# Kernel optimization log

Measured on AMD Instinct MI355X. Metric: run time of the kernel, lower is better.

Reference implementation:

```python
import jax, jax.numpy as jnp
import numpy as np

NEG_SLOPE = 0.01  # torch F.leaky_relu default
EPS = 1e-12


def setup_inputs() -> dict:
    key = jax.random.key(0)
    k1, k2, k3, k4 = jax.random.split(key, 4)
    num_nodes, in_f, out_f, num_edges = 50000, 128, 128, 600000
    x = jax.random.normal(k1, (num_nodes, in_f), dtype=jnp.float32)
    edge_index = jax.random.randint(k2, (2, num_edges), 0, num_nodes, dtype=jnp.int64)
    # xavier_uniform for W:[out,in]
    limit = float(np.sqrt(6.0 / (in_f + out_f)))
    W = jax.random.uniform(k3, (out_f, in_f), dtype=jnp.float32, minval=-limit, maxval=limit)
    a = jax.random.uniform(k4, (2 * out_f,), dtype=jnp.float32, minval=0.0, maxval=1.0)
    return {"x": x, "edge_index": edge_index, "W": W, "a": a}


def reference(x, edge_index, W, a):
    num_nodes = x.shape[0]
    out_f = W.shape[0]
    # add self loops
    loops = jnp.arange(num_nodes, dtype=edge_index.dtype)
    src = jnp.concatenate([edge_index[0], loops])
    dst = jnp.concatenate([edge_index[1], loops])
    messages = x @ W.T                      # [N, F_out]
    # cat([h_src,h_dst]) @ a == h_src @ a[:F] + h_dst @ a[F:] (avoids materializing concat)
    s_src = messages @ a[:out_f]            # [N]
    s_dst = messages @ a[out_f:]            # [N]
    e_ij = jax.nn.leaky_relu(s_src[src] + s_dst[dst], negative_slope=NEG_SLOPE)  # [E]
    w = jnp.exp(e_ij)                       # unnormalized edge weights
    denom = jax.ops.segment_sum(w, dst, num_segments=num_nodes)
    denom = jnp.maximum(denom, EPS)
    weighted = w[:, None] * messages[src]   # [E, F_out]
    agg = jax.ops.segment_sum(weighted, dst, num_segments=num_nodes)
    return agg / denom[:, None]
```

## Files before the change

### kernel.cpp

```cpp
#include <hip/hip_runtime.h>

#define NEG_SLOPE 0.01f
#define CAP 64

typedef __attribute__((ext_vector_type(8))) short bf16x8;
typedef __attribute__((ext_vector_type(4))) float f32x4;

static __device__ __forceinline__ unsigned short f2bf(float f) {
  unsigned u = __float_as_uint(f);
  u += 0x7fffu + ((u >> 16) & 1u);
  return (unsigned short)(u >> 16);
}

__global__ __launch_bounds__(256) void k_setup(const float* __restrict__ W,
                                               const float* __restrict__ a,
                                               unsigned short* __restrict__ Wb,
                                               float* __restrict__ p_lo,
                                               float* __restrict__ p_hi,
                                               int* __restrict__ counts, int N, int nz) {
  int b = blockIdx.x;
  int t = threadIdx.x;
  if (b < nz) {
    int i = b * 256 + t;
    if (i < N) counts[i] = 0;
  } else if (b < nz + 64) {
    int i = (b - nz) * 256 + t;
    Wb[i] = f2bf(W[i]);
  } else {
    if (t < 128) {
      float lo = 0.f, hi = 0.f;
#pragma unroll 8
      for (int f = 0; f < 128; ++f) {
        float w = W[f * 128 + t];
        lo += w * a[f];
        hi += w * a[128 + f];
      }
      p_lo[t] = lo;
      p_hi[t] = hi;
    }
  }
}

__global__ __launch_bounds__(256) void k_msg(const float* __restrict__ x,
                                             const float* __restrict__ p_lo,
                                             const float* __restrict__ p_hi,
                                             const unsigned short* __restrict__ Wb,
                                             unsigned short* __restrict__ msgs,
                                             float* __restrict__ s_src,
                                             float* __restrict__ s_dst, int N) {
  int wave = (blockIdx.x * 256 + threadIdx.x) >> 6;
  int lane = threadIdx.x & 63;
  int base = wave * 16;
  if (base >= N) return;
  int q = lane >> 4, r = lane & 15;
  int node = base + r;
  const float* xrow = x + (size_t)node * 128 + q * 8;
  const float4* pl = (const float4*)p_lo;
  const float4* ph = (const float4*)p_hi;
  bf16x8 afrag[4];
  float lo = 0.f, hi = 0.f;
#pragma unroll
  for (int c = 0; c < 4; ++c) {
    float4 v0 = *(const float4*)(xrow + c * 32);
    float4 v1 = *(const float4*)(xrow + c * 32 + 4);
    int fi = q * 2 + c * 8;
    float4 a0 = pl[fi], a1 = pl[fi + 1];
    float4 b0 = ph[fi], b1 = ph[fi + 1];
    lo += v0.x * a0.x + v0.y * a0.y + v0.z * a0.z + v0.w * a0.w
        + v1.x * a1.x + v1.y * a1.y + v1.z * a1.z + v1.w * a1.w;
    hi += v0.x * b0.x + v0.y * b0.y + v0.z * b0.z + v0.w * b0.w
        + v1.x * b1.x + v1.y * b1.y + v1.z * b1.z + v1.w * b1.w;
    bf16x8 f;
    f[0] = (short)f2bf(v0.x); f[1] = (short)f2bf(v0.y);
    f[2] = (short)f2bf(v0.z); f[3] = (short)f2bf(v0.w);
    f[4] = (short)f2bf(v1.x); f[5] = (short)f2bf(v1.y);
    f[6] = (short)f2bf(v1.z); f[7] = (short)f2bf(v1.w);
    afrag[c] = f;
  }
  lo += __shfl_xor(lo, 16); lo += __shfl_xor(lo, 32);
  hi += __shfl_xor(hi, 16); hi += __shfl_xor(hi, 32);
  if (q == 0) { s_src[node] = lo; s_dst[node] = hi; }
#pragma unroll
  for (int ft = 0; ft < 8; ++ft) {
    const unsigned short* wrow = Wb + (size_t)(ft * 16 + r) * 128 + q * 8;
    f32x4 acc = {0.f, 0.f, 0.f, 0.f};
#pragma unroll
    for (int c = 0; c < 4; ++c) {
      bf16x8 bfrag = *(const bf16x8*)(wrow + c * 32);
      acc = __builtin_amdgcn_mfma_f32_16x16x32_bf16(afrag[c], bfrag, acc, 0, 0, 0);
    }
#pragma unroll
    for (int rr = 0; rr < 4; ++rr) {
      int n2 = base + q * 4 + rr;
      msgs[(size_t)n2 * 128 + ft * 16 + r] = f2bf(acc[rr]);
    }
  }
}

__global__ __launch_bounds__(256) void k_scatter(const int* __restrict__ ei,
                                                 const float* __restrict__ s_src,
                                                 const float* __restrict__ s_dst,
                                                 int* __restrict__ counts,
                                                 int2* __restrict__ edges, int E) {
  int e2 = blockIdx.x * 256 + threadIdx.x;
  int e = e2 * 2;
  if (e >= E) return;
  int2 srcp = *(const int2*)(ei + e);
  int2 dstp = *(const int2*)(ei + E + e);
  {
    float z = s_src[srcp.x] + s_dst[dstp.x];
    z = z > 0.f ? z : NEG_SLOPE * z;
    float w = expf(z);
    int pos = atomicAdd(&counts[dstp.x], 1);
    if (pos < CAP) edges[(size_t)dstp.x * CAP + pos] = make_int2(srcp.x, __float_as_int(w));
  }
  if (e + 1 < E) {
    float z = s_src[srcp.y] + s_dst[dstp.y];
    z = z > 0.f ? z : NEG_SLOPE * z;
    float w = expf(z);
    int pos = atomicAdd(&counts[dstp.y], 1);
    if (pos < CAP) edges[(size_t)dstp.y * CAP + pos] = make_int2(srcp.y, __float_as_int(w));
  }
}

__global__ __launch_bounds__(256) void k_agg(const unsigned short* __restrict__ msgs,
                                             const int* __restrict__ counts,
                                             const int2* __restrict__ edges,
                                             const float* __restrict__ s_src,
                                             const float* __restrict__ s_dst,
                                             float* __restrict__ out, int N) {
  int wave = (blockIdx.x * 256 + threadIdx.x) >> 6;
  int lane = threadIdx.x & 63;
  if (wave >= N) return;
  int node = wave;
  int g = lane >> 4;
  int r = lane & 15;
  float zs = s_src[node] + s_dst[node];
  zs = zs > 0.f ? zs : NEG_SLOPE * zs;
  float wself = expf(zs);
  float wg = (g == 0) ? wself : 0.f;
  float denom = wg;
  float acc[8];
  {
    const uint4* mrow = (const uint4*)(msgs + (size_t)node * 128);
    uint4 m = mrow[r];
    unsigned mm[4] = {m.x, m.y, m.z, m.w};
#pragma unroll
    for (int c = 0; c < 4; ++c) {
      acc[2 * c]     = wg * __uint_as_float(mm[c] << 16);
      acc[2 * c + 1] = wg * __uint_as_float(mm[c] & 0xffff0000u);
    }
  }
  int cnt = counts[node];
  cnt = cnt < CAP ? cnt : CAP;
  const int2* bucket = edges + (size_t)node * CAP;
  int nIter = (cnt + 7) >> 3;
  for (int it = 0; it < nIter; ++it) {
    int k0 = it * 8 + g;
    int k1 = k0 + 4;
    bool v0 = k0 < cnt, v1 = k1 < cnt;
    int2 e0 = bucket[v0 ? k0 : 0];
    int2 e1 = bucket[v1 ? k1 : 0];
    float w0 = v0 ? __int_as_float(e0.y) : 0.f;
    float w1 = v1 ? __int_as_float(e1.y) : 0.f;
    uint4 m0 = ((const uint4*)(msgs + (size_t)e0.x * 128))[r];
    uint4 m1 = ((const uint4*)(msgs + (size_t)e1.x * 128))[r];
    unsigned a0[4] = {m0.x, m0.y, m0.z, m0.w};
    unsigned a1[4] = {m1.x, m1.y, m1.z, m1.w};
#pragma unroll
    for (int c = 0; c < 4; ++c) {
      acc[2 * c]     += w0 * __uint_as_float(a0[c] << 16);
      acc[2 * c + 1] += w0 * __uint_as_float(a0[c] & 0xffff0000u);
      acc[2 * c]     += w1 * __uint_as_float(a1[c] << 16);
      acc[2 * c + 1] += w1 * __uint_as_float(a1[c] & 0xffff0000u);
    }
    denom += w0 + w1;
  }
#pragma unroll
  for (int mask = 16; mask < 64; mask <<= 1) {
#pragma unroll
    for (int j = 0; j < 8; ++j) acc[j] += __shfl_xor(acc[j], mask);
    denom += __shfl_xor(denom, mask);
  }
  if (g == 0) {
    float inv = 1.f / fmaxf(denom, 1e-12f);
    float4 o0 = {acc[0] * inv, acc[1] * inv, acc[2] * inv, acc[3] * inv};
    float4 o1 = {acc[4] * inv, acc[5] * inv, acc[6] * inv, acc[7] * inv};
    float4* orow = (float4*)(out + (size_t)node * 128);
    orow[r * 2] = o0;
    orow[r * 2 + 1] = o1;
  }
}

extern "C" void kernel_launch(void* const* d_in, const int* in_sizes, int n_in,
                              void* d_out, int out_size, void* d_ws, size_t ws_size,
                              hipStream_t stream) {
  const float* x = (const float*)d_in[0];
  const int* ei = (const int*)d_in[1];
  const float* W = (const float*)d_in[2];
  const float* a = (const float*)d_in[3];
  float* out = (float*)d_out;
  int N = in_sizes[0] / 128;
  int E = in_sizes[1] / 2;

  char* ws = (char*)d_ws;
  size_t off = 0;
  auto alloc = [&](size_t bytes) {
    off = (off + 255) & ~(size_t)255;
    void* p = ws + off;
    off += bytes;
    return p;
  };
  unsigned short* msgs = (unsigned short*)alloc((size_t)N * 128 * 2);
  float* s_src = (float*)alloc((size_t)N * 4);
  float* s_dst = (float*)alloc((size_t)N * 4);
  float* p_lo = (float*)alloc(512);
  float* p_hi = (float*)alloc(512);
  unsigned short* Wb = (unsigned short*)alloc(128 * 128 * 2);
  int* counts = (int*)alloc((size_t)N * 4);
  int2* edges = (int2*)alloc((size_t)N * CAP * 8);

  int nz = (N + 255) / 256;
  int waves = (N + 15) / 16;
  k_setup<<<nz + 64 + 1, 256, 0, stream>>>(W, a, Wb, p_lo, p_hi, counts, N, nz);
  k_msg<<<(waves + 3) / 4, 256, 0, stream>>>(x, p_lo, p_hi, Wb, msgs, s_src, s_dst, N);
  int e2 = (E + 1) / 2;
  k_scatter<<<(e2 + 255) / 256, 256, 0, stream>>>(ei, s_src, s_dst, counts, edges, E);
  k_agg<<<(N + 3) / 4, 256, 0, stream>>>(msgs, counts, edges, s_src, s_dst, out, N);
}
```

Before: 165.9 us.

## Move edge weight computation into aggregation and shrink edge buckets to indices

The scatter kernel now stores only the source index per bucket slot instead of an (index, weight) pair, which halves the bucket storage and its write and read traffic. The attention weight (gather s_src, leaky relu, exp) is recomputed inside the aggregation kernel per edge. Scatter no longer depends on s_src and s_dst, so it is launched before the message kernel. The cost is an extra random s_src gather and an exp per edge in the aggregation loop.

After: 164.6 us. No clear change (-0.8%).

```diff
diff --git a/kernel.cpp b/kernel.cpp
--- a/kernel.cpp
+++ b/kernel.cpp
@@ -98,34 +98,24 @@
 }
 
 __global__ __launch_bounds__(256) void k_scatter(const int* __restrict__ ei,
-                                                 const float* __restrict__ s_src,
-                                                 const float* __restrict__ s_dst,
                                                  int* __restrict__ counts,
-                                                 int2* __restrict__ edges, int E) {
+                                                 unsigned* __restrict__ edges, int E) {
   int e2 = blockIdx.x * 256 + threadIdx.x;
   int e = e2 * 2;
   if (e >= E) return;
   int2 srcp = *(const int2*)(ei + e);
   int2 dstp = *(const int2*)(ei + E + e);
-  {
-    float z = s_src[srcp.x] + s_dst[dstp.x];
-    z = z > 0.f ? z : NEG_SLOPE * z;
-    float w = expf(z);
-    int pos = atomicAdd(&counts[dstp.x], 1);
-    if (pos < CAP) edges[(size_t)dstp.x * CAP + pos] = make_int2(srcp.x, __float_as_int(w));
-  }
+  int pos0 = atomicAdd(&counts[dstp.x], 1);
+  if (pos0 < CAP) edges[(size_t)dstp.x * CAP + pos0] = (unsigned)srcp.x;
   if (e + 1 < E) {
-    float z = s_src[srcp.y] + s_dst[dstp.y];
-    z = z > 0.f ? z : NEG_SLOPE * z;
-    float w = expf(z);
-    int pos = atomicAdd(&counts[dstp.y], 1);
-    if (pos < CAP) edges[(size_t)dstp.y * CAP + pos] = make_int2(srcp.y, __float_as_int(w));
+    int pos1 = atomicAdd(&counts[dstp.y], 1);
+    if (pos1 < CAP) edges[(size_t)dstp.y * CAP + pos1] = (unsigned)srcp.y;
   }
 }
 
 __global__ __launch_bounds__(256) void k_agg(const unsigned short* __restrict__ msgs,
                                              const int* __restrict__ counts,
-                                             const int2* __restrict__ edges,
+                                             const unsigned* __restrict__ edges,
                                              const float* __restrict__ s_src,
                                              const float* __restrict__ s_dst,
                                              float* __restrict__ out, int N) {
@@ -135,7 +125,8 @@
   int node = wave;
   int g = lane >> 4;
   int r = lane & 15;
-  float zs = s_src[node] + s_dst[node];
+  float sdn = s_dst[node];
+  float zs = s_src[node] + sdn;
   zs = zs > 0.f ? zs : NEG_SLOPE * zs;
   float wself = expf(zs);
   float wg = (g == 0) ? wself : 0.f;
@@ -153,18 +144,22 @@
   }
   int cnt = counts[node];
   cnt = cnt < CAP ? cnt : CAP;
-  const int2* bucket = edges + (size_t)node * CAP;
+  const unsigned* bucket = edges + (size_t)node * CAP;
   int nIter = (cnt + 7) >> 3;
   for (int it = 0; it < nIter; ++it) {
     int k0 = it * 8 + g;
     int k1 = k0 + 4;
     bool v0 = k0 < cnt, v1 = k1 < cnt;
-    int2 e0 = bucket[v0 ? k0 : 0];
-    int2 e1 = bucket[v1 ? k1 : 0];
-    float w0 = v0 ? __int_as_float(e0.y) : 0.f;
-    float w1 = v1 ? __int_as_float(e1.y) : 0.f;
-    uint4 m0 = ((const uint4*)(msgs + (size_t)e0.x * 128))[r];
-    uint4 m1 = ((const uint4*)(msgs + (size_t)e1.x * 128))[r];
+    unsigned e0 = bucket[v0 ? k0 : 0];
+    unsigned e1 = bucket[v1 ? k1 : 0];
+    uint4 m0 = ((const uint4*)(msgs + (size_t)e0 * 128))[r];
+    uint4 m1 = ((const uint4*)(msgs + (size_t)e1 * 128))[r];
+    float ss0 = s_src[e0];
+    float ss1 = s_src[e1];
+    float z0 = ss0 + sdn; z0 = z0 > 0.f ? z0 : NEG_SLOPE * z0;
+    float z1 = ss1 + sdn; z1 = z1 > 0.f ? z1 : NEG_SLOPE * z1;
+    float w0 = v0 ? expf(z0) : 0.f;
+    float w1 = v1 ? expf(z1) : 0.f;
     unsigned a0[4] = {m0.x, m0.y, m0.z, m0.w};
     unsigned a1[4] = {m1.x, m1.y, m1.z, m1.w};
 #pragma unroll
@@ -218,13 +213,12 @@
   float* p_hi = (float*)alloc(512);
   unsigned short* Wb = (unsigned short*)alloc(128 * 128 * 2);
   int* counts = (int*)alloc((size_t)N * 4);
-  int2* edges = (int2*)alloc((size_t)N * CAP * 8);
+  unsigned* edges = (unsigned*)alloc((size_t)N * CAP * 4);
 
   int nz = (N + 255) / 256;
   int waves = (N + 15) / 16;
   k_setup<<<nz + 64 + 1, 256, 0, stream>>>(W, a, Wb, p_lo, p_hi, counts, N, nz);
+  k_scatter<<<((E + 1) / 2 + 255) / 256, 256, 0, stream>>>(ei, counts, edges, E);
   k_msg<<<(waves + 3) / 4, 256, 0, stream>>>(x, p_lo, p_hi, Wb, msgs, s_src, s_dst, N);
-  int e2 = (E + 1) / 2;
-  k_scatter<<<(e2 + 255) / 256, 256, 0, stream>>>(ei, s_src, s_dst, counts, edges, E);
   k_agg<<<(N + 3) / 4, 256, 0, stream>>>(msgs, counts, edges, s_src, s_dst, out, N);
 }
```
